# Optimization experiments

Hardware: AMD Instinct MI355X
Metric: run time of the kernel (lower is better)

The kernel has to match this reference:

```python
import jax, jax.numpy as jnp
import numpy as np

W = 64          # word_embedding_size
ES = 64         # entity_embedding_size
H = 4           # head_num
DH = W // H
K = 3           # convolution_num
NW, NQ, NE, NR = 50000, 20000, 200000, 100000
LQ, LR, EP, B = 8, 16, 500000, 1024
D = ES + W      # propagated entity feature dim


def _mhsa_mean(x, Wq, bq, Wk, bk, Wv, bv, Wo, bo):
    # x: [N, L, W] -> [N, W]; standard multi-head self-attention then mean over L
    N, L, _ = x.shape
    q = (x @ Wq + bq).reshape(N, L, H, DH)
    k = (x @ Wk + bk).reshape(N, L, H, DH)
    v = (x @ Wv + bv).reshape(N, L, H, DH)
    s = jnp.einsum('nlhd,nmhd->nhlm', q, k) / jnp.sqrt(jnp.asarray(DH, x.dtype))
    a = jax.nn.softmax(s, axis=-1)
    o = jnp.einsum('nhlm,nmhd->nlhd', a, v).reshape(N, L, W)
    return (o @ Wo + bo).mean(axis=1)


def setup_inputs() -> dict:
    key = jax.random.key(0)
    ks = jax.random.split(key, 20)
    f = jnp.float32
    inp = {
        'word_emb': jax.random.normal(ks[0], (NW, W), f) * 0.02,
        'entity_emb': jax.random.normal(ks[1], (NE, ES), f) * 0.02,
        'Wq': jax.random.normal(ks[2], (W, W), f) * (1.0 / np.sqrt(W)),
        'bq': jnp.zeros((W,), f),
        'Wk': jax.random.normal(ks[3], (W, W), f) * (1.0 / np.sqrt(W)),
        'bk': jnp.zeros((W,), f),
        'Wv': jax.random.normal(ks[4], (W, W), f) * (1.0 / np.sqrt(W)),
        'bv': jnp.zeros((W,), f),
        'Wo': jax.random.normal(ks[5], (W, W), f) * (1.0 / np.sqrt(W)),
        'bo': jnp.zeros((W,), f),
        'review_words': jax.random.randint(ks[6], (NR, LR), 0, NW),
        'query_words_graph': jax.random.randint(ks[7], (NQ, LQ), 0, NW),
        'profile_dst': jax.random.randint(ks[8], (NR,), 0, NE),
        'pur_src': jax.random.randint(ks[9], (EP,), 0, NE),
        'pur_dst': jax.random.randint(ks[10], (EP,), 0, NE),
        'pur_qid': jax.random.randint(ks[11], (EP,), 0, NQ),
        'users': jax.random.randint(ks[12], (B,), 0, NE),
        'items': jax.random.randint(ks[13], (B,), 0, NE),
        'negs': jax.random.randint(ks[14], (B,), 0, NE),
        'query_words': jax.random.randint(ks[15], (B, LQ), 0, NW),
    }
    return inp


def reference(word_emb, entity_emb, Wq, bq, Wk, bk, Wv, bv, Wo, bo,
              review_words, query_words_graph, profile_dst,
              pur_src, pur_dst, pur_qid, users, items, negs, query_words):
    seg = jax.ops.segment_sum
    attn = lambda x: _mhsa_mean(x, Wq, bq, Wk, bk, Wv, bv, Wo, bo)
    we = word_emb.at[0].set(0.0)  # padding_idx=0

    # composes: word -> review / query (mailbox attention reduce)
    rev_h = attn(we[review_words])              # [NR, W]
    q_h = attn(we[query_words_graph])           # [NQ, W]
    q_e0 = jnp.concatenate([jnp.zeros((NQ, ES), we.dtype), q_h], axis=-1)  # [NQ, D]

    # profiles: review -> entity, mean by in-degree
    deg_p = jnp.clip(seg(jnp.ones((NR,), we.dtype), profile_dst, num_segments=NE), 1.0)[:, None]
    prof = seg(rev_h, profile_dst, num_segments=NE) / deg_p   # [NE, W]
    e = jnp.concatenate([entity_emb, prof], axis=-1)          # e_0: [NE, D]

    # deg_i = out_deg(purchased) + out_deg(purchased_by), clamped
    ones_e = jnp.ones((EP,), we.dtype)
    deg_i = jnp.clip(seg(ones_e, pur_src, num_segments=NE)
                     + seg(ones_e, pur_dst, num_segments=NE), 1.0)[:, None]
    inv = 1.0 / jnp.sqrt(deg_i)                               # [NE, 1]

    es = [e]
    for _ in range(K):
        msg = e * inv                                         # e_k / sqrt(deg_i)
        m_pur = e[pur_src] + q_e0[pur_qid] * inv[pur_src]     # msg_u_i UDF
        nxt = seg(m_pur, pur_dst, num_segments=NE) \
            + seg(msg[pur_dst], pur_src, num_segments=NE)     # purchased_by (reverse)
        e = nxt * inv
        es.append(e)
    efin = sum(es) / (K + 1)                                  # [NE, D]

    # batch scoring
    u = efin[users]
    qb = attn(we[query_words])                                # [B, W]
    p = u + jnp.concatenate([jnp.zeros((B, ES), we.dtype), qb], axis=-1)
    pos = jnp.sum(p * efin[items], axis=-1)
    neg = jnp.sum(p * efin[negs], axis=-1)
    loss = -jnp.mean(jax.nn.log_sigmoid(pos - neg))           # BPR loss
    return loss
```

## Files before the change

kernel.cpp:

```cpp
#include <hip/hip_runtime.h>
#include <hip/hip_fp8.h>
#include <cstdint>

#define CDIV(a,b) (((a)+(b)-1)/(b))

typedef __attribute__((ext_vector_type(8))) short bf16x8;
typedef __attribute__((ext_vector_type(4))) float f32x4;
typedef __attribute__((ext_vector_type(8))) float f32x8;
typedef __attribute__((ext_vector_type(4))) _Float16 half4;
typedef __attribute__((ext_vector_type(8))) _Float16 half8;

#define QK_SCALE 32.0f
#define SCORE_SCALE (0.25f / (QK_SCALE * QK_SCALE))
#define EXP2_C (SCORE_SCALE * 1.44269504089f)

#define ES_SCALE 64.0f

__device__ __forceinline__ float bf2f(short s) {
    return __builtin_bit_cast(float, ((unsigned)(unsigned short)s) << 16);
}
__device__ __forceinline__ short rtne(float f) {
    const unsigned u = __builtin_bit_cast(unsigned, f);
    return (short)((u + 0x7fffu + ((u >> 16) & 1u)) >> 16);
}
__device__ __forceinline__ unsigned pack2r(float lo, float hi) {
    return (unsigned)(unsigned short)rtne(lo) | ((unsigned)(unsigned short)rtne(hi) << 16);
}
__device__ __forceinline__ float fp8tof(unsigned char b) {
    __hip_fp8_e4m3 t; t.__x = b; return (float)t;
}
__device__ __forceinline__ unsigned char ftofp8(float f) {
    __hip_fp8_e4m3 t(f); return t.__x;
}
__device__ __forceinline__ f32x8 fp8x8tof32(long v) {
    union { long l; unsigned char b[8]; } u; u.l = v;
    f32x8 r;
    #pragma unroll
    for (int j = 0; j < 8; ++j) r[j] = fp8tof(u.b[j]);
    return r;
}
__device__ __forceinline__ long f32x8tofp8(f32x8 a) {
    union { long l; unsigned char b[8]; } u;
    #pragma unroll
    for (int j = 0; j < 8; ++j) u.b[j] = ftofp8(a[j]);
    return u.l;
}

template<int CTRL>
__device__ __forceinline__ float dpp_add(float x) {
    const int t = __builtin_amdgcn_update_dpp(0, __builtin_bit_cast(int, x),
                                              CTRL, 0xf, 0xf, true);
    return x + __builtin_bit_cast(float, t);
}
__device__ __forceinline__ float rowsum16(float x) {
    x = dpp_add<0x108>(x);
    x = dpp_add<0x104>(x);
    x = dpp_add<0x102>(x);
    x = dpp_add<0x101>(x);
    return x;
}


__device__ __forceinline__ void prep_body(int bid,
    const float* __restrict__ we, const short* __restrict__ Wt,
    const float* __restrict__ bq, const float* __restrict__ bk,
    const float* __restrict__ bv, unsigned char* __restrict__ WQKV, int NW)
{
    const int wave = threadIdx.x >> 6;
    const int lane = threadIdx.x & 63;
    const int quad = lane >> 4;
    const int lm   = lane & 15;
    const int ntiles = CDIV(NW, 16);

    bf16x8 bfr[3][4][2];
    #pragma unroll
    for (int p = 0; p < 3; ++p)
        #pragma unroll
        for (int nt = 0; nt < 4; ++nt)
            #pragma unroll
            for (int kh = 0; kh < 2; ++kh)
                bfr[p][nt][kh] = *(const bf16x8*)(Wt + ((p*64 + nt*16 + lm)*64) + kh*32 + quad*8);
    float bias[3][4];
    #pragma unroll
    for (int nt = 0; nt < 4; ++nt) {
        bias[0][nt] = bq[nt*16 + lm];
        bias[1][nt] = bk[nt*16 + lm];
        bias[2][nt] = bv[nt*16 + lm];
    }

    #pragma unroll
    for (int t = 0; t < 4; ++t) {
        const int tile = (bid*4 + wave)*4 + t;
        if (tile >= ntiles) return;
        const int wb = tile*16;
        int w = wb + lm;
        if (w >= NW) w = NW - 1;
        const float* xr = we + (size_t)w*64;
        union { unsigned u[4]; bf16x8 v; } a0, a1;
        const float4 f0 = *(const float4*)(xr + quad*8);
        const float4 f1 = *(const float4*)(xr + quad*8 + 4);
        const float4 f2 = *(const float4*)(xr + 32 + quad*8);
        const float4 f3 = *(const float4*)(xr + 32 + quad*8 + 4);
        a0.u[0] = pack2r(f0.x, f0.y); a0.u[1] = pack2r(f0.z, f0.w);
        a0.u[2] = pack2r(f1.x, f1.y); a0.u[3] = pack2r(f1.z, f1.w);
        a1.u[0] = pack2r(f2.x, f2.y); a1.u[1] = pack2r(f2.z, f2.w);
        a1.u[2] = pack2r(f3.x, f3.y); a1.u[3] = pack2r(f3.z, f3.w);
        if (w == 0) {
            a0.u[0]=0u; a0.u[1]=0u; a0.u[2]=0u; a0.u[3]=0u;
            a1.u[0]=0u; a1.u[1]=0u; a1.u[2]=0u; a1.u[3]=0u;
        }
        #pragma unroll
        for (int p = 0; p < 3; ++p) {
            #pragma unroll
            for (int nt = 0; nt < 4; ++nt) {
                f32x4 c = {bias[p][nt], bias[p][nt], bias[p][nt], bias[p][nt]};
                c = __builtin_amdgcn_mfma_f32_16x16x32_bf16(a0.v, bfr[p][nt][0], c, 0, 0, 0);
                c = __builtin_amdgcn_mfma_f32_16x16x32_bf16(a1.v, bfr[p][nt][1], c, 0, 0, 0);
                #pragma unroll
                for (int r = 0; r < 4; ++r) {
                    const int w2 = wb + quad*4 + r;
                    if (w2 < NW) {
                        unsigned char* rowo = WQKV + (size_t)w2*192;
                        const int base = (p == 2) ? 128 : (p == 0) ? 64 : 0;
                        rowo[base + nt*16 + lm] = ftofp8(c[r] * QK_SCALE);
                    }
                }
            }
        }
    }
}

__device__ __forceinline__ void fill_body(int bid,
    const int* __restrict__ src, const int* __restrict__ dst,
    const int* __restrict__ qid,
    int* __restrict__ curC, int2* __restrict__ cmb2, int EP)
{
    const int t = bid*256 + threadIdx.x;
    if (t >= EP) return;
    const int s = src[t], d = dst[t];
    const int p1 = atomicAdd(&curC[d], 1);
    int2 e1; e1.x = s; e1.y = qid[t];
    cmb2[p1] = e1;
    const int p2 = atomicAdd(&curC[s], 1);
    int2 e2; e2.x = d | (int)0x80000000; e2.y = 0;
    cmb2[p2] = e2;
}

__device__ __forceinline__ void expand_body(int bid, int nb, unsigned targ,
    const int* __restrict__ slist, const int* __restrict__ pn,
    const int* __restrict__ offC, const int* __restrict__ endC,
    const int2* __restrict__ cmb2, unsigned* __restrict__ lev,
    int* __restrict__ dl1, int* __restrict__ dn1,
    int* __restrict__ dl2, int* __restrict__ dn2)
{
    const int n = *pn;
    const int stride = nb * 256;
    for (int t = bid*256 + threadIdx.x; t < n; t += stride) {
        const int v = slist[t];
        const int b0 = offC[v], e0 = endC[v];
        for (int i = b0; i < e0; ++i) {
            const int u = cmb2[i].x & 0x7fffffff;
            const unsigned old = atomicMax(&lev[u], targ);
            if (old < targ) {
                dl1[atomicAdd(dn1, 1)] = u;
                if (dl2) dl2[atomicAdd(dn2, 1)] = u;
            }
        }
    }
}

__device__ __forceinline__ void finalize_body(int bid,
    const float* __restrict__ emb, const float* __restrict__ prof,
    unsigned char* __restrict__ e8, float* __restrict__ inv,
    const unsigned* __restrict__ deg_p, const unsigned* __restrict__ cntC, int NE)
{
    const int t = bid*256 + threadIdx.x;
    const int v = t >> 5;
    if (v >= NE) return;
    const int c = (t & 31) * 4;
    float4 ev;
    if (c < 64) {
        ev = *(const float4*)&emb[(size_t)v*64 + c];
    } else {
        ev = *(const float4*)&prof[(size_t)v*64 + (c - 64)];
        const unsigned dp = deg_p[v];
        const float r = 1.0f / (float)(dp > 1u ? dp : 1u);
        ev.x *= r; ev.y *= r; ev.z *= r; ev.w *= r;
    }
    union { unsigned u; unsigned char b[4]; } pk;
    pk.b[0] = ftofp8(ev.x * ES_SCALE);
    pk.b[1] = ftofp8(ev.y * ES_SCALE);
    pk.b[2] = ftofp8(ev.z * ES_SCALE);
    pk.b[3] = ftofp8(ev.w * ES_SCALE);
    *(unsigned*)&e8[(size_t)v*128 + c] = pk.u;
    if (c == 0) {
        const unsigned di = cntC[v];
        inv[v] = 1.0f / sqrtf((float)(di > 1u ? di : 1u));
    }
}

__device__ __forceinline__ void qconst_body(int bid, int nb,
    const _Float16* __restrict__ q_h16, const float* __restrict__ inv,
    const int* __restrict__ offC, const int* __restrict__ endC,
    const int2* __restrict__ cmb2,
    const int* __restrict__ list, const int* __restrict__ pn,
    _Float16* __restrict__ qc)
{
    const int n = *pn;
    const int stride = nb * 256;
    for (int t = bid*256 + threadIdx.x; (t >> 3) < n; t += stride) {
        const int v = list[t >> 3];
        const int c = (t & 7) * 8;
        f32x8 a = {0.f,0.f,0.f,0.f,0.f,0.f,0.f,0.f};
        const int b0 = offC[v], e0 = endC[v];
        for (int i = b0; i < e0; ++i) {
            const int2 e = cmb2[i];
            if (e.x >= 0) {
                const float invs = inv[e.x];
                const half8 qh = *(const half8*)&q_h16[(size_t)e.y*64 + c];
                a += __builtin_convertvector(qh, f32x8) * invs;
            }
        }
        a *= ES_SCALE;
        *(half8*)&qc[(size_t)v*64 + c] = __builtin_convertvector(a, half8);
    }
}

__device__ __forceinline__ void gather_body(int bid,
    const unsigned char* __restrict__ e8, const int* __restrict__ users,
    const int* __restrict__ items, const int* __restrict__ negs,
    float* __restrict__ acc, int B)
{
    const int t = bid*256 + threadIdx.x;
    const int r = t >> 4;
    if (r >= 3*B) return;
    const int c = (t & 15) * 8;
    const int which = r / B, b = r - which*B;
    const int idx = (which == 0) ? users[b] : (which == 1) ? items[b] : negs[b];
    const long ev = *(const long*)&e8[(size_t)idx*128 + c];
    f32x8 a = *(const f32x8*)&acc[(size_t)r*128 + c];
    a += fp8x8tof32(ev);
    *(f32x8*)&acc[(size_t)r*128 + c] = a;
}

__device__ __forceinline__ void prop_list_body(int bid, int nb,
    const unsigned char* __restrict__ e_cur, const _Float16* __restrict__ qc,
    const float* __restrict__ inv,
    const int* __restrict__ offC, const int* __restrict__ endC,
    const int2* __restrict__ cmb2,
    const int* __restrict__ list, const int* __restrict__ pn,
    unsigned char* __restrict__ e_nxt)
{
    const int n = *pn;
    const int stride = nb * 256;
    for (int t = bid*256 + threadIdx.x; (t >> 4) < n; t += stride) {
        const int v = list[t >> 4];
        const int c = (t & 15) * 8;
        f32x8 a = {0.f,0.f,0.f,0.f,0.f,0.f,0.f,0.f};
        if (c >= 64) {
            const half8 q = *(const half8*)&qc[(size_t)v*64 + (c - 64)];
            a = __builtin_convertvector(q, f32x8);
        }
        const int b0 = offC[v], e0 = endC[v];
        int un = (b0 < e0) ? cmb2[b0].x : 0;
        for (int i = b0; i < e0; ++i) {
            const int uc = un;
            if (i + 1 < e0) un = cmb2[i + 1].x;
            const int u = uc & 0x7fffffff;
            const long es = *(const long*)&e_cur[(size_t)u*128 + c];
            const float w = (uc < 0) ? inv[u] : 1.0f;
            a += fp8x8tof32(es) * w;
        }
        a *= inv[v];
        *(long*)&e_nxt[(size_t)v*128 + c] = f32x8tofp8(a);
    }
}

struct TileRegs { int4 v0; long qf[4], kf[4]; };

__device__ __forceinline__ void load_tile(
    const unsigned char* __restrict__ WQKV, int w, int quad, TileRegs& t)
{
    const unsigned char* row = WQKV + (size_t)w * 192;
    t.v0 = *(const int4*)(row + 128 + quad*16);
    #pragma unroll
    for (int h = 0; h < 4; ++h) {
        if (quad < 2) {
            t.kf[h] = *(const long*)(row +      h*16 + quad*8);
            t.qf[h] = *(const long*)(row + 64 + h*16 + quad*8);
        } else {
            t.kf[h] = 0; t.qf[h] = 0;
        }
    }
}

template<int L, int MODE>
__device__ __forceinline__ void attn_body(
    unsigned char* __restrict__ smem,
    const unsigned char* __restrict__ WQKV, const int* __restrict__ words,
    const short* __restrict__ WoT, const float* __restrict__ bo,
    int N, void* __restrict__ outp, const int* __restrict__ sidx, int bid)
{
    constexpr int SPT = 16 / L;
    constexpr int SB  = 16 * SPT;
    unsigned char (*v_s)[16*80] = (unsigned char (*)[16*80])smem;
    float (*pbar_s)[64]         = (float (*)[64])(smem + 5120);
    float (*mo_s)[68]           = (float (*)[68])(smem + 6144);

    const int wave = threadIdx.x >> 6;
    const int lane = threadIdx.x & 63;
    const int quad = lane >> 4;
    const int lm   = lane & 15;
    const int tok_total = N * L;
    const float invL = 1.0f / ((float)L * QK_SCALE);

    int wid[4];
    #pragma unroll
    for (int t = 0; t < 4; ++t) {
        int tg = (bid*16 + wave*4 + t)*16 + lm;
        if (tg >= tok_total) tg = tok_total - 1;
        wid[t] = words[tg];
    }

    TileRegs cur, nxt;
    load_tile(WQKV, wid[0], quad, cur);

    #pragma unroll
    for (int ti = 0; ti < 4; ++ti) {
        if (ti < 3) load_tile(WQKV, wid[ti+1], quad, nxt);

        *(int4*)&v_s[wave][lm*80 + quad*16] = cur.v0;

        const bool mvalid = (SPT == 1) ? true : ((quad >> 1) == ((lm >> 3) & 1));

        #pragma unroll
        for (int h = 0; h < 4; ++h) {
            const f32x4 s4 = __builtin_amdgcn_mfma_f32_16x16x32_fp8_fp8(
                cur.kf[h], cur.qf[h], (f32x4){0.f,0.f,0.f,0.f}, 0, 0, 0);
            float sv0 = s4[0], sv1 = s4[1], sv2 = s4[2], sv3 = s4[3];
            if (!mvalid) { sv0 = sv1 = sv2 = sv3 = -3.0e38f; }
            float p0 = __builtin_amdgcn_exp2f(sv0*EXP2_C),
                  p1 = __builtin_amdgcn_exp2f(sv1*EXP2_C),
                  p2 = __builtin_amdgcn_exp2f(sv2*EXP2_C),
                  p3 = __builtin_amdgcn_exp2f(sv3*EXP2_C);
            float sm = p0+p1+p2+p3;
            sm += __shfl_xor(sm, 16, 64);
            sm += __shfl_xor(sm, 32, 64);
            const float rinv = __builtin_amdgcn_rcpf(sm);
            p0 *= rinv; p1 *= rinv; p2 *= rinv; p3 *= rinv;
            p0 = rowsum16(p0); p1 = rowsum16(p1);
            p2 = rowsum16(p2); p3 = rowsum16(p3);
            if (lm == 0) {
                pbar_s[wave][h*16 + quad*4 + 0] = p0 * invL;
                pbar_s[wave][h*16 + quad*4 + 1] = p1 * invL;
                pbar_s[wave][h*16 + quad*4 + 2] = p2 * invL;
                pbar_s[wave][h*16 + quad*4 + 3] = p3 * invL;
            }
        }

        #pragma unroll
        for (int s = 0; s < SPT; ++s) {
            f32x4 pb[4];
            #pragma unroll
            for (int j = 0; j < 4; ++j)
                pb[j] = *(const f32x4*)&pbar_s[wave][quad*16 + j*4];
            float o = 0.f;
            #pragma unroll
            for (int j2 = 0; j2 < L; ++j2) {
                const int m = s*L + j2;
                o += pb[m >> 2][m & 3] * fp8tof(v_s[wave][m*80 + lane]);
            }
            mo_s[(wave*4+ti)*SPT + s][lane] = o;
        }

        if (ti < 3) {
            cur.v0 = nxt.v0;
            #pragma unroll
            for (int h = 0; h < 4; ++h) { cur.qf[h] = nxt.qf[h]; cur.kf[h] = nxt.kf[h]; }
        }
    }
    __syncthreads();

    const int col = wave*16 + lm;
    const short* bT = WoT + col*64;
    const bf16x8 b0 = *(const bf16x8*)(bT + quad*8);
    const bf16x8 b1 = *(const bf16x8*)(bT + 32 + quad*8);
    const float boc = bo[col];
    #pragma unroll
    for (int rt = 0; rt < SPT; ++rt) {
        const float* ar = mo_s[rt*16 + lm];
        const float4 fA0 = *(const float4*)(ar + quad*8);
        const float4 fA1 = *(const float4*)(ar + quad*8 + 4);
        const float4 fA2 = *(const float4*)(ar + 32 + quad*8);
        const float4 fA3 = *(const float4*)(ar + 32 + quad*8 + 4);
        union { unsigned u[4]; bf16x8 v; } a0, a1;
        a0.u[0] = pack2r(fA0.x, fA0.y); a0.u[1] = pack2r(fA0.z, fA0.w);
        a0.u[2] = pack2r(fA1.x, fA1.y); a0.u[3] = pack2r(fA1.z, fA1.w);
        a1.u[0] = pack2r(fA2.x, fA2.y); a1.u[1] = pack2r(fA2.z, fA2.w);
        a1.u[2] = pack2r(fA3.x, fA3.y); a1.u[3] = pack2r(fA3.z, fA3.w);
        f32x4 c = {boc, boc, boc, boc};
        c = __builtin_amdgcn_mfma_f32_16x16x32_bf16(a0.v, b0, c, 0, 0, 0);
        c = __builtin_amdgcn_mfma_f32_16x16x32_bf16(a1.v, b1, c, 0, 0, 0);
        #pragma unroll
        for (int r = 0; r < 4; ++r) {
            const int seq = bid*SB + rt*16 + quad*4 + r;
            if (seq < N) {
                if (MODE == 0)
                    ((float*)outp)[(size_t)seq*64 + col] = c[r];
                else if (MODE == 1)
                    atomicAdd(&((float*)outp)[(size_t)sidx[seq]*64 + col], c[r]);
                else
                    ((_Float16*)outp)[(size_t)seq*64 + col] = (_Float16)c[r];
            }
        }
    }
}


__global__ __launch_bounds__(256) void misc_kernel(
    const int* __restrict__ src, const int* __restrict__ dst,
    unsigned* __restrict__ cntC, int EP,
    const int* __restrict__ pdst, unsigned* __restrict__ deg_p, int NR,
    const float* __restrict__ Wo, short* __restrict__ WoT,
    const float* __restrict__ Wq, const float* __restrict__ Wk,
    const float* __restrict__ Wv, short* __restrict__ Wt,
    const int* __restrict__ users, const int* __restrict__ items,
    const int* __restrict__ negs, int B, unsigned* __restrict__ lev,
    int* __restrict__ listS, int* __restrict__ list2, int* __restrict__ list1,
    int* __restrict__ nS, int* __restrict__ n2, int* __restrict__ n1)
{
    const int t = blockIdx.x*256 + threadIdx.x;
    if (t < EP) {
        const int s = src[t], d = dst[t];
        atomicAdd(&cntC[d], 1u); atomicAdd(&cntC[s], 1u);
    }
    if (t < NR) atomicAdd(&deg_p[pdst[t]], 1u);
    if (t < 4096) {
        const int j = t >> 6, k = t & 63;
        WoT[j*64 + k] = rtne(Wo[k*64 + j]);
    }
    if (t < 3*4096) {
        const int p = t >> 12, n = (t >> 6) & 63, k = t & 63;
        const float* W = (p==0) ? Wq : (p==1) ? Wk : Wv;
        Wt[t] = rtne(W[k*64 + n]);
    }
    if (t < 3*B) {
        const int which = t / B, b = t - which*B;
        const int v = (which == 0) ? users[b] : (which == 1) ? items[b] : negs[b];
        const unsigned old = atomicMax(&lev[v], 3u);
        if (old < 3u) {
            listS[atomicAdd(nS, 1)] = v;
            list2[atomicAdd(n2, 1)] = v;
            list1[atomicAdd(n1, 1)] = v;
        }
    }
}

#define SCAN_CHUNK 2048

__device__ __forceinline__ void scan_reduce_body(int b,
    const unsigned* __restrict__ cnt, unsigned* __restrict__ part, int n)
{
    const int base = b * SCAN_CHUNK;
    unsigned s = 0;
    #pragma unroll
    for (int i = 0; i < 8; ++i) {
        const int idx = base + i*256 + threadIdx.x;
        if (idx < n) s += cnt[idx];
    }
    #pragma unroll
    for (int off = 1; off < 64; off <<= 1) s += __shfl_xor(s, off, 64);
    __shared__ unsigned wsum[4];
    if ((threadIdx.x & 63) == 0) wsum[threadIdx.x >> 6] = s;
    __syncthreads();
    if (threadIdx.x == 0) part[b] = wsum[0]+wsum[1]+wsum[2]+wsum[3];
}

__global__ __launch_bounds__(256) void mega_scan_prep(
    const unsigned* __restrict__ cnt, unsigned* __restrict__ part, int n, int NB,
    const float* __restrict__ we, const short* __restrict__ Wt,
    const float* __restrict__ bq, const float* __restrict__ bk,
    const float* __restrict__ bv, unsigned char* __restrict__ WQKV, int NW)
{
    const int b = blockIdx.x;
    if (b < NB) scan_reduce_body(b, cnt, part, n);
    else        prep_body(b - NB, we, Wt, bq, bk, bv, WQKV, NW);
}

__global__ __launch_bounds__(1024) void scan_part_kernel(
    unsigned* __restrict__ part, int NB)
{
    __shared__ unsigned a[1024];
    const int t = threadIdx.x;
    a[t] = (t < NB) ? part[t] : 0u;
    __syncthreads();
    for (int d = 1; d < 1024; d <<= 1) {
        const unsigned xa = (t >= d) ? a[t-d] : 0u;
        __syncthreads();
        a[t] += xa;
        __syncthreads();
    }
    if (t < NB) part[t] = (t > 0) ? a[t-1] : 0u;
}

__global__ __launch_bounds__(256) void scan_final_kernel(
    const unsigned* __restrict__ cnt, const unsigned* __restrict__ part,
    int* __restrict__ off, int* __restrict__ cur, int n)
{
    const int b = blockIdx.x;
    __shared__ unsigned v[SCAN_CHUNK];
    __shared__ unsigned tsum[256];
    const int base = b * SCAN_CHUNK;
    const int t = threadIdx.x;
    #pragma unroll
    for (int i = 0; i < 8; ++i) {
        const int idx = base + i*256 + t;
        v[i*256 + t] = (idx < n) ? cnt[idx] : 0u;
    }
    __syncthreads();
    unsigned s = 0;
    #pragma unroll
    for (int i = 0; i < 8; ++i) s += v[t*8 + i];
    tsum[t] = s;
    __syncthreads();
    for (int d = 1; d < 256; d <<= 1) {
        const unsigned x = (t >= d) ? tsum[t-d] : 0u;
        __syncthreads();
        tsum[t] += x;
        __syncthreads();
    }
    unsigned run = ((t > 0) ? tsum[t-1] : 0u) + part[b];
    #pragma unroll
    for (int i = 0; i < 8; ++i) {
        const int idx = base + t*8 + i;
        if (idx < n) { off[idx] = (int)run; cur[idx] = (int)run; run += v[t*8+i]; }
    }
}

__global__ __launch_bounds__(256) void mega_attn(
    const unsigned char* __restrict__ WQKV,
    const int* __restrict__ src, const int* __restrict__ dst,
    const int* __restrict__ qid, int* __restrict__ curC,
    int2* __restrict__ cmb2, int EP, int nbF,
    const int* __restrict__ w1, int N1, float* __restrict__ o1,
    const int* __restrict__ sidx1, int nb1,
    const int* __restrict__ w2, int N2, _Float16* __restrict__ o2, int nb2,
    const int* __restrict__ w3, int N3, float* __restrict__ o3,
    const short* __restrict__ WoT, const float* __restrict__ bo)
{
    __shared__ __align__(16) unsigned char smem[6144 + 32*68*4];
    const int b = blockIdx.x;
    if (b < nb1) {
        attn_body<16,1>(smem, WQKV, w1, WoT, bo, N1, o1, sidx1, b);
        return;
    }
    const int b2 = b - nb1;
    if (b2 < nb2) {
        attn_body<8,2>(smem, WQKV, w2, WoT, bo, N2, o2, nullptr, b2);
        return;
    }
    const int b3 = b2 - nb2;
    if (b3 < nbF) {
        fill_body(b3, src, dst, qid, curC, cmb2, EP);
        return;
    }
    attn_body<8,0>(smem, WQKV, w3, WoT, bo, N3, o3, nullptr, b3 - nbF);
}

__global__ __launch_bounds__(256) void expand_kernel(
    unsigned targ, const int* __restrict__ slist, const int* __restrict__ pn,
    const int* __restrict__ offC, const int* __restrict__ endC,
    const int2* __restrict__ cmb2, unsigned* __restrict__ lev,
    int* __restrict__ dl1, int* __restrict__ dn1,
    int* __restrict__ dl2, int* __restrict__ dn2)
{
    expand_body(blockIdx.x, gridDim.x, targ, slist, pn, offC, endC, cmb2, lev,
                dl1, dn1, dl2, dn2);
}

__global__ __launch_bounds__(256) void mega_final(
    const int* __restrict__ list2, const int* __restrict__ n2,
    const int* __restrict__ offC, const int* __restrict__ endC,
    const int2* __restrict__ cmb2, unsigned* __restrict__ lev,
    int* __restrict__ list1, int* __restrict__ n1,
    const float* __restrict__ emb, const float* __restrict__ prof,
    unsigned char* __restrict__ e8, float* __restrict__ inv,
    const unsigned* __restrict__ deg_p, const unsigned* __restrict__ cntC, int NE)
{
    const int b = blockIdx.x;
    if (b < 256)
        expand_body(b, 256, 1u, list2, n2, offC, endC, cmb2, lev,
                    list1, n1, nullptr, nullptr);
    else
        finalize_body(b - 256, emb, prof, e8, inv, deg_p, cntC, NE);
}

__global__ __launch_bounds__(256) void mega_qg(
    const _Float16* __restrict__ q_h16, const float* __restrict__ inv,
    const int* __restrict__ offC, const int* __restrict__ endC,
    const int2* __restrict__ cmb2,
    const int* __restrict__ list1, const int* __restrict__ n1,
    _Float16* __restrict__ qc,
    const unsigned char* __restrict__ e8, const int* __restrict__ users,
    const int* __restrict__ items, const int* __restrict__ negs,
    float* __restrict__ acc, int B)
{
    const int b = blockIdx.x;
    if (b < 512) qconst_body(b, 512, q_h16, inv, offC, endC, cmb2, list1, n1, qc);
    else         gather_body(b - 512, e8, users, items, negs, acc, B);
}

__global__ __launch_bounds__(256) void mega_pg(
    const unsigned char* __restrict__ e_cur, const _Float16* __restrict__ qc,
    const float* __restrict__ inv,
    const int* __restrict__ offC, const int* __restrict__ endC,
    const int2* __restrict__ cmb2,
    const int* __restrict__ list2, const int* __restrict__ n2,
    unsigned char* __restrict__ e_nxt,
    const int* __restrict__ users, const int* __restrict__ items,
    const int* __restrict__ negs, float* __restrict__ acc, int B)
{
    const int b = blockIdx.x;
    if (b < 512) prop_list_body(b, 512, e_cur, qc, inv, offC, endC, cmb2,
                                list2, n2, e_nxt);
    else         gather_body(b - 512, e_cur, users, items, negs, acc, B);
}

__global__ __launch_bounds__(256) void prop_list_kernel(
    const unsigned char* __restrict__ e_cur, const _Float16* __restrict__ qc,
    const float* __restrict__ inv,
    const int* __restrict__ offC, const int* __restrict__ endC,
    const int2* __restrict__ cmb2,
    const int* __restrict__ list, const int* __restrict__ pn,
    unsigned char* __restrict__ e_nxt)
{
    prop_list_body(blockIdx.x, gridDim.x, e_cur, qc, inv, offC, endC, cmb2,
                   list, pn, e_nxt);
}

__global__ __launch_bounds__(256) void prop_batch_kernel(
    const unsigned char* __restrict__ e_cur, const _Float16* __restrict__ qc,
    const float* __restrict__ inv,
    const int* __restrict__ offC, const int* __restrict__ endC,
    const int2* __restrict__ cmb2,
    const int* __restrict__ users, const int* __restrict__ items,
    const int* __restrict__ negs, float* __restrict__ acc, int B)
{
    const int t = blockIdx.x*256 + threadIdx.x;
    const int r = t >> 4;
    if (r >= 3*B) return;
    const int c = (t & 15) * 8;
    const int which = r / B, b = r - which*B;
    const int v = (which == 0) ? users[b] : (which == 1) ? items[b] : negs[b];
    f32x8 a = {0.f,0.f,0.f,0.f,0.f,0.f,0.f,0.f};
    if (c >= 64) {
        const half8 q = *(const half8*)&qc[(size_t)v*64 + (c - 64)];
        a = __builtin_convertvector(q, f32x8);
    }
    const int b0 = offC[v], e0 = endC[v];
    int un = (b0 < e0) ? cmb2[b0].x : 0;
    for (int i = b0; i < e0; ++i) {
        const int uc = un;
        if (i + 1 < e0) un = cmb2[i + 1].x;
        const int u = uc & 0x7fffffff;
        const long es = *(const long*)&e_cur[(size_t)u*128 + c];
        const float w = (uc < 0) ? inv[u] : 1.0f;
        a += fp8x8tof32(es) * w;
    }
    a *= inv[v];
    a += fp8x8tof32(*(const long*)&e_cur[(size_t)v*128 + c]);
    f32x8 ac = *(const f32x8*)&acc[(size_t)r*128 + c];
    ac += a;
    *(f32x8*)&acc[(size_t)r*128 + c] = ac;
}

__global__ __launch_bounds__(128) void loss_kernel(
    const float* __restrict__ acc, const float* __restrict__ qb,
    float* __restrict__ out, int B, float invB)
{
    const int b = blockIdx.x, d = threadIdx.x;
    const float u = acc[(size_t)b*128 + d] * (0.25f / ES_SCALE);
    const float p = u + (d >= 64 ? qb[(size_t)b*64 + (d - 64)] : 0.f);
    const float ei = acc[(size_t)(B + b)*128 + d];
    const float en = acc[(size_t)(2*B + b)*128 + d];
    float x = p * (ei - en) * (0.25f / ES_SCALE);
    #pragma unroll
    for (int off = 1; off < 64; off <<= 1) x += __shfl_xor(x, off, 64);
    __shared__ float wred[2];
    if ((threadIdx.x & 63) == 0) wred[threadIdx.x >> 6] = x;
    __syncthreads();
    if (threadIdx.x == 0) {
        const float xx = wred[0] + wred[1];
        const float ls = fminf(xx, 0.f) - log1pf(expf(-fabsf(xx)));
        atomicAdd(out, -ls * invB);
    }
}

extern "C" void kernel_launch(void* const* d_in, const int* in_sizes, int n_in,
                              void* d_out, int out_size, void* d_ws, size_t ws_size,
                              hipStream_t stream)
{
    const float* word_emb        = (const float*)d_in[0];
    const float* entity_emb      = (const float*)d_in[1];
    const float* Wq = (const float*)d_in[2];  const float* bq = (const float*)d_in[3];
    const float* Wk = (const float*)d_in[4];  const float* bk = (const float*)d_in[5];
    const float* Wv = (const float*)d_in[6];  const float* bv = (const float*)d_in[7];
    const float* Wo = (const float*)d_in[8];  const float* bo = (const float*)d_in[9];
    const int* review_words      = (const int*)d_in[10];
    const int* query_words_graph = (const int*)d_in[11];
    const int* profile_dst       = (const int*)d_in[12];
    const int* pur_src           = (const int*)d_in[13];
    const int* pur_dst           = (const int*)d_in[14];
    const int* pur_qid           = (const int*)d_in[15];
    const int* users             = (const int*)d_in[16];
    const int* items             = (const int*)d_in[17];
    const int* negs              = (const int*)d_in[18];
    const int* query_words       = (const int*)d_in[19];

    const int NW = in_sizes[0]  / 64;
    const int NE = in_sizes[1]  / 64;
    const int NR = in_sizes[10] / 16;
    const int NQ = in_sizes[11] / 8;
    const int EP = in_sizes[13];
    const int B  = in_sizes[16];
    const int NB = CDIV(NE, SCAN_CHUNK);

    char* ws = (char*)d_ws;
    size_t off = 0;
    auto alloc = [&](size_t bytes) -> char* {
        char* q = ws + off; off += (bytes + 255) & ~(size_t)255; return q;
    };
    float*         prof  = (float*)         alloc((size_t)NE*64*4);
    unsigned char* e8A   = (unsigned char*) alloc((size_t)NE*128);
    unsigned char* e8B   = (unsigned char*) alloc((size_t)NE*128);
    _Float16*      q_h16 = (_Float16*)      alloc((size_t)NQ*64*2);
    float*         qb    = (float*)         alloc((size_t)B*64*4);
    float*         acc   = (float*)         alloc((size_t)3*B*128*4);
    unsigned*  deg_p   = (unsigned*) alloc((size_t)NE*4);
    unsigned*  cntC    = (unsigned*) alloc((size_t)NE*4);
    unsigned*  lev     = (unsigned*) alloc((size_t)NE*4);
    int*       fcnt    = (int*)      alloc(256);
    int*       offC    = (int*)      alloc((size_t)NE*4);
    int*       curC    = (int*)      alloc((size_t)NE*4);
    int2*      cmb2    = (int2*)     alloc((size_t)2*EP*8);
    int*       listS   = (int*)      alloc((size_t)3*B*4);
    int*       list2   = (int*)      alloc((size_t)NE*4);
    int*       list1   = (int*)      alloc((size_t)NE*4);
    float*     inv     = (float*)    alloc((size_t)NE*4);
    unsigned*  part    = (unsigned*) alloc((size_t)NB*4);
    short*     WoT     = (short*)    alloc((size_t)64*64*2);
    short*     Wt      = (short*)    alloc((size_t)3*64*64*2);

    if (off > ws_size) return;

    unsigned char* WQKV = e8A;
    _Float16* qc = (_Float16*)prof;
    int* nS = fcnt; int* n2 = fcnt + 1; int* n1 = fcnt + 2;

    const size_t zlen = (size_t)((char*)fcnt - (char*)deg_p) + 256;
    hipMemsetAsync(deg_p, 0, zlen, stream);
    hipMemsetAsync(prof,  0, (size_t)NE*64*4, stream);
    hipMemsetAsync(acc,   0, (size_t)3*B*128*4, stream);
    hipMemsetAsync(d_out, 0, (size_t)out_size*4, stream);

    misc_kernel<<<CDIV(EP, 256), 256, 0, stream>>>(pur_src, pur_dst, cntC, EP,
        profile_dst, deg_p, NR, Wo, WoT, Wq, Wk, Wv, Wt,
        users, items, negs, B, lev, listS, list2, list1, nS, n2, n1);

    const int nbP = CDIV(CDIV(NW, 16), 16);
    mega_scan_prep<<<NB + nbP, 256, 0, stream>>>(cntC, part, NE, NB,
        word_emb, Wt, bq, bk, bv, WQKV, NW);
    scan_part_kernel<<<1, 1024, 0, stream>>>(part, NB);
    scan_final_kernel<<<NB, 256, 0, stream>>>(cntC, part, offC, curC, NE);

    const int nbF = CDIV(EP, 256);
    const int nb1 = CDIV(NR, 16), nb2 = CDIV(NQ, 32), nb3 = CDIV(B, 32);
    mega_attn<<<nb1 + nb2 + nbF + nb3, 256, 0, stream>>>(WQKV,
        pur_src, pur_dst, pur_qid, curC, cmb2, EP, nbF,
        review_words, NR, prof, profile_dst, nb1,
        query_words_graph, NQ, q_h16, nb2,
        query_words, B, qb, WoT, bo);

    expand_kernel<<<64, 256, 0, stream>>>(2u, listS, nS, offC, curC, cmb2, lev,
        list2, n2, list1, n1);

    mega_final<<<256 + CDIV(NE*32, 256), 256, 0, stream>>>(
        list2, n2, offC, curC, cmb2, lev, list1, n1,
        entity_emb, prof, e8A, inv, deg_p, cntC, NE);

    mega_qg<<<512 + CDIV(3*B*16, 256), 256, 0, stream>>>(
        q_h16, inv, offC, curC, cmb2, list1, n1, qc,
        e8A, users, items, negs, acc, B);

    prop_list_kernel<<<2048, 256, 0, stream>>>(e8A, qc, inv,
        offC, curC, cmb2, list1, n1, e8B);

    mega_pg<<<512 + CDIV(3*B*16, 256), 256, 0, stream>>>(
        e8B, qc, inv, offC, curC, cmb2, list2, n2, e8A,
        users, items, negs, acc, B);

    prop_batch_kernel<<<CDIV(3*B*16, 256), 256, 0, stream>>>(e8A, qc, inv,
        offC, curC, cmb2, users, items, negs, acc, B);

    loss_kernel<<<B, 128, 0, stream>>>(acc, qb, (float*)d_out, B, 1.0f / (float)B);
}
```

Baseline: 498.9 us.

## Fuse query-constant computation into first propagation pass and use nontemporal CSR stores

Merges the separate qconst pass, which computes per-node query message sums, into the first propagation kernel. Each node's edge list is now walked once instead of twice, and one kernel launch is removed. The query lanes compute qc inline, write it out for the later hop, and add it into the propagated value. The CSR fill now writes its 64-bit entries with nontemporal stores. The fused pass makes lanes with c<64 idle during the query loads, which may add divergence.

```diff
diff --git a/kernel.cpp b/kernel.cpp
--- a/kernel.cpp
+++ b/kernel.cpp
@@ -139,11 +139,11 @@
     if (t >= EP) return;
     const int s = src[t], d = dst[t];
     const int p1 = atomicAdd(&curC[d], 1);
-    int2 e1; e1.x = s; e1.y = qid[t];
-    cmb2[p1] = e1;
+    const long e1 = (long)(unsigned)s | ((long)(unsigned)qid[t] << 32);
+    __builtin_nontemporal_store(e1, (long*)(cmb2 + p1));
     const int p2 = atomicAdd(&curC[s], 1);
-    int2 e2; e2.x = d | (int)0x80000000; e2.y = 0;
-    cmb2[p2] = e2;
+    const long e2 = (long)(unsigned)(d | (int)0x80000000);
+    __builtin_nontemporal_store(e2, (long*)(cmb2 + p2));
 }
 
 __device__ __forceinline__ void expand_body(int bid, int nb, unsigned targ,
@@ -199,33 +199,6 @@
     }
 }
 
-__device__ __forceinline__ void qconst_body(int bid, int nb,
-    const _Float16* __restrict__ q_h16, const float* __restrict__ inv,
-    const int* __restrict__ offC, const int* __restrict__ endC,
-    const int2* __restrict__ cmb2,
-    const int* __restrict__ list, const int* __restrict__ pn,
-    _Float16* __restrict__ qc)
-{
-    const int n = *pn;
-    const int stride = nb * 256;
-    for (int t = bid*256 + threadIdx.x; (t >> 3) < n; t += stride) {
-        const int v = list[t >> 3];
-        const int c = (t & 7) * 8;
-        f32x8 a = {0.f,0.f,0.f,0.f,0.f,0.f,0.f,0.f};
-        const int b0 = offC[v], e0 = endC[v];
-        for (int i = b0; i < e0; ++i) {
-            const int2 e = cmb2[i];
-            if (e.x >= 0) {
-                const float invs = inv[e.x];
-                const half8 qh = *(const half8*)&q_h16[(size_t)e.y*64 + c];
-                a += __builtin_convertvector(qh, f32x8) * invs;
-            }
-        }
-        a *= ES_SCALE;
-        *(half8*)&qc[(size_t)v*64 + c] = __builtin_convertvector(a, half8);
-    }
-}
-
 __device__ __forceinline__ void gather_body(int bid,
     const unsigned char* __restrict__ e8, const int* __restrict__ users,
     const int* __restrict__ items, const int* __restrict__ negs,
@@ -241,6 +214,43 @@
     f32x8 a = *(const f32x8*)&acc[(size_t)r*128 + c];
     a += fp8x8tof32(ev);
     *(f32x8*)&acc[(size_t)r*128 + c] = a;
+}
+
+__device__ __forceinline__ void prop1_body(int bid, int nb,
+    const unsigned char* __restrict__ e_cur, const _Float16* __restrict__ q_h16,
+    const float* __restrict__ inv,
+    const int* __restrict__ offC, const int* __restrict__ endC,
+    const int2* __restrict__ cmb2,
+    const int* __restrict__ list, const int* __restrict__ pn,
+    unsigned char* __restrict__ e_nxt, _Float16* __restrict__ qc)
+{
+    const int n = *pn;
+    const int stride = nb * 256;
+    for (int t = bid*256 + threadIdx.x; (t >> 4) < n; t += stride) {
+        const int v = list[t >> 4];
+        const int c = (t & 15) * 8;
+        const bool qlane = (c >= 64);
+        f32x8 a  = {0.f,0.f,0.f,0.f,0.f,0.f,0.f,0.f};
+        f32x8 qa = {0.f,0.f,0.f,0.f,0.f,0.f,0.f,0.f};
+        const int b0 = offC[v], e0 = endC[v];
+        for (int i = b0; i < e0; ++i) {
+            const int2 e = cmb2[i];
+            const int u = e.x & 0x7fffffff;
+            const float w = (e.x < 0) ? inv[u] : 1.0f;
+            a += fp8x8tof32(*(const long*)&e_cur[(size_t)u*128 + c]) * w;
+            if (e.x >= 0 && qlane) {
+                const half8 qh = *(const half8*)&q_h16[(size_t)e.y*64 + (c - 64)];
+                qa += __builtin_convertvector(qh, f32x8) * inv[u];
+            }
+        }
+        if (qlane) {
+            qa *= ES_SCALE;
+            *(half8*)&qc[(size_t)v*64 + (c - 64)] = __builtin_convertvector(qa, half8);
+            a += qa;
+        }
+        a *= inv[v];
+        *(long*)&e_nxt[(size_t)v*128 + c] = f32x8tofp8(a);
+    }
 }
 
 __device__ __forceinline__ void prop_list_body(int bid, int nb,
@@ -595,19 +605,20 @@
         finalize_body(b - 256, emb, prof, e8, inv, deg_p, cntC, NE);
 }
 
-__global__ __launch_bounds__(256) void mega_qg(
-    const _Float16* __restrict__ q_h16, const float* __restrict__ inv,
+__global__ __launch_bounds__(256) void mega_prop1(
+    const unsigned char* __restrict__ e_cur, const _Float16* __restrict__ q_h16,
+    const float* __restrict__ inv,
     const int* __restrict__ offC, const int* __restrict__ endC,
     const int2* __restrict__ cmb2,
     const int* __restrict__ list1, const int* __restrict__ n1,
-    _Float16* __restrict__ qc,
-    const unsigned char* __restrict__ e8, const int* __restrict__ users,
-    const int* __restrict__ items, const int* __restrict__ negs,
-    float* __restrict__ acc, int B)
+    unsigned char* __restrict__ e_nxt, _Float16* __restrict__ qc,
+    const int* __restrict__ users, const int* __restrict__ items,
+    const int* __restrict__ negs, float* __restrict__ acc, int B)
 {
     const int b = blockIdx.x;
-    if (b < 512) qconst_body(b, 512, q_h16, inv, offC, endC, cmb2, list1, n1, qc);
-    else         gather_body(b - 512, e8, users, items, negs, acc, B);
+    if (b < 2048) prop1_body(b, 2048, e_cur, q_h16, inv, offC, endC, cmb2,
+                             list1, n1, e_nxt, qc);
+    else          gather_body(b - 2048, e_cur, users, items, negs, acc, B);
 }
 
 __global__ __launch_bounds__(256) void mega_pg(
@@ -624,18 +635,6 @@
     if (b < 512) prop_list_body(b, 512, e_cur, qc, inv, offC, endC, cmb2,
                                 list2, n2, e_nxt);
     else         gather_body(b - 512, e_cur, users, items, negs, acc, B);
-}
-
-__global__ __launch_bounds__(256) void prop_list_kernel(
-    const unsigned char* __restrict__ e_cur, const _Float16* __restrict__ qc,
-    const float* __restrict__ inv,
-    const int* __restrict__ offC, const int* __restrict__ endC,
-    const int2* __restrict__ cmb2,
-    const int* __restrict__ list, const int* __restrict__ pn,
-    unsigned char* __restrict__ e_nxt)
-{
-    prop_list_body(blockIdx.x, gridDim.x, e_cur, qc, inv, offC, endC, cmb2,
-                   list, pn, e_nxt);
 }
 
 __global__ __launch_bounds__(256) void prop_batch_kernel(
@@ -788,12 +787,9 @@
         list2, n2, offC, curC, cmb2, lev, list1, n1,
         entity_emb, prof, e8A, inv, deg_p, cntC, NE);
 
-    mega_qg<<<512 + CDIV(3*B*16, 256), 256, 0, stream>>>(
-        q_h16, inv, offC, curC, cmb2, list1, n1, qc,
-        e8A, users, items, negs, acc, B);
-
-    prop_list_kernel<<<2048, 256, 0, stream>>>(e8A, qc, inv,
-        offC, curC, cmb2, list1, n1, e8B);
+    mega_prop1<<<2048 + CDIV(3*B*16, 256), 256, 0, stream>>>(
+        e8A, q_h16, inv, offC, curC, cmb2, list1, n1, e8B, qc,
+        users, items, negs, acc, B);
 
     mega_pg<<<512 + CDIV(3*B*16, 256), 256, 0, stream>>>(
         e8B, qc, inv, offC, curC, cmb2, list2, n2, e8A,
```

New measurement: 503.1 us. No clear change (+0.8%).
